# Kernel optimization log

Hardware: AMD Instinct MI355X
Metric: run time of the kernel (lower is better)

The kernel has to match this reference:

```python
import jax, jax.numpy as jnp
import numpy as np

LN_EPS = 1e-5

def setup_inputs() -> dict:
    key = jax.random.key(0)
    k1, k2, k3 = jax.random.split(key, 3)
    B, S, D = 4, 4096, 768
    seq_feat = jax.random.normal(k1, (B, S, D), dtype=jnp.float32)
    msa_feat = jax.random.normal(k2, (B, S, D), dtype=jnp.float32)
    ln_gamma = jnp.ones((2 * D,), dtype=jnp.float32)
    ln_beta = jnp.zeros((2 * D,), dtype=jnp.float32)
    # torch init zeroes gate weight; use small random weights for a non-degenerate test
    gate_w = jax.random.normal(k3, (2, 2 * D), dtype=jnp.float32) * 0.02
    gate_b = jnp.zeros((2,), dtype=jnp.float32)
    return {"seq_feat": seq_feat, "msa_feat": msa_feat, "ln_gamma": ln_gamma,
            "ln_beta": ln_beta, "gate_w": gate_w, "gate_b": gate_b}

def reference(seq_feat, msa_feat, ln_gamma, ln_beta, gate_w, gate_b):
    # h: [B, S, 2D]
    h = jnp.concatenate([seq_feat, msa_feat], axis=-1)
    mean = jnp.mean(h, axis=-1, keepdims=True)
    var = jnp.mean(jnp.square(h - mean), axis=-1, keepdims=True)
    hn = (h - mean) * jax.lax.rsqrt(var + LN_EPS) * ln_gamma + ln_beta
    # dropout in eval mode = identity
    logits = jnp.einsum('bsd,kd->bsk', hn, gate_w) + gate_b  # [B, S, 2]
    w = jax.nn.softmax(logits, axis=-1)
    return w[..., 0:1] * seq_feat + w[..., 1:2] * msa_feat
```

## Files before the change

### kernel.cpp

```cpp
#include <hip/hip_runtime.h>

#define LN_EPS 1e-5f
#define D 768
#define D4 192
#define TWO_D 1536


__global__ __launch_bounds__(64) void setup_kernel(
    const float* __restrict__ gamma, const float* __restrict__ beta,
    const float* __restrict__ gate_w, const float* __restrict__ gate_b,
    float* __restrict__ ws)
{
    const int lane = threadIdx.x;
    const float4* g4  = (const float4*)gamma;
    const float4* b4  = (const float4*)beta;
    const float4* w04 = (const float4*)gate_w;
    const float4* w14 = (const float4*)(gate_w + TWO_D);
    float4* P04 = (float4*)ws;
    float4* P14 = (float4*)(ws + TWO_D);

    float C0 = 0.f, C1 = 0.f, E0 = 0.f, E1 = 0.f;
    #pragma unroll
    for (int j = 0; j < 6; ++j) {
        const int idx = j * 64 + lane;
        float4 g = g4[idx], bb = b4[idx], w0 = w04[idx], w1 = w14[idx];
        float4 p0, p1;
        p0.x = g.x * w0.x; p0.y = g.y * w0.y; p0.z = g.z * w0.z; p0.w = g.w * w0.w;
        p1.x = g.x * w1.x; p1.y = g.y * w1.y; p1.z = g.z * w1.z; p1.w = g.w * w1.w;
        P04[idx] = p0;
        P14[idx] = p1;
        C0 += p0.x + p0.y + p0.z + p0.w;
        C1 += p1.x + p1.y + p1.z + p1.w;
        E0 += bb.x * w0.x + bb.y * w0.y + bb.z * w0.z + bb.w * w0.w;
        E1 += bb.x * w1.x + bb.y * w1.y + bb.z * w1.z + bb.w * w1.w;
    }
    #pragma unroll
    for (int off = 32; off > 0; off >>= 1) {
        C0 += __shfl_xor(C0, off, 64);
        C1 += __shfl_xor(C1, off, 64);
        E0 += __shfl_xor(E0, off, 64);
        E1 += __shfl_xor(E1, off, 64);
    }
    if (lane == 0) {
        float* c = ws + 2 * TWO_D;
        c[0] = C0;
        c[1] = C1;
        c[2] = E0 + gate_b[0];
        c[3] = E1 + gate_b[1];
    }
}

__global__ __launch_bounds__(256) void fused_gate_kernel(
    const float* __restrict__ seq, const float* __restrict__ msa,
    const float* __restrict__ ws, float* __restrict__ out, int nrows)
{
    const int wave = threadIdx.x >> 6;
    const int lane = threadIdx.x & 63;
    const int row = blockIdx.x * 4 + wave;
    if (row >= nrows) return;

    const float4* s4 = (const float4*)(seq + (size_t)row * D);
    const float4* m4 = (const float4*)(msa + (size_t)row * D);
    const float4* P04 = (const float4*)ws;
    const float4* P14 = (const float4*)(ws + TWO_D);

    float4 s[3], m[3];
    #pragma unroll
    for (int j = 0; j < 3; ++j) {
        s[j] = s4[j * 64 + lane];
        m[j] = m4[j * 64 + lane];
    }
    const float4 cst = *(const float4*)(ws + 2 * TWO_D);

    float su = 0.f, sq = 0.f, a0 = 0.f, a1 = 0.f;
    #pragma unroll
    for (int j = 0; j < 6; ++j) {
        const int idx = (j < 3) ? (j * 64 + lane) : (D4 + (j - 3) * 64 + lane);
        const float4 p0 = P04[idx];
        const float4 p1 = P14[idx];
        const float4 h = (j < 3) ? s[j] : m[j - 3];
        su += h.x + h.y + h.z + h.w;
        sq += h.x * h.x + h.y * h.y + h.z * h.z + h.w * h.w;
        a0 += h.x * p0.x + h.y * p0.y + h.z * p0.z + h.w * p0.w;
        a1 += h.x * p1.x + h.y * p1.y + h.z * p1.z + h.w * p1.w;
    }
    #pragma unroll
    for (int off = 32; off > 0; off >>= 1) {
        su += __shfl_xor(su, off, 64);
        sq += __shfl_xor(sq, off, 64);
        a0 += __shfl_xor(a0, off, 64);
        a1 += __shfl_xor(a1, off, 64);
    }

    const float inv_n = 1.f / (float)TWO_D;
    const float mean = su * inv_n;
    const float var  = fmaxf(sq * inv_n - mean * mean, 0.f);
    const float rstd = rsqrtf(var + LN_EPS);
    const float l0 = rstd * (a0 - mean * cst.x) + cst.z;
    const float l1 = rstd * (a1 - mean * cst.y) + cst.w;
    const float mx = fmaxf(l0, l1);
    const float e0 = __expf(l0 - mx), e1 = __expf(l1 - mx);
    const float inv = 1.f / (e0 + e1);
    const float w0s = e0 * inv, w1s = e1 * inv;

    float4* o4 = (float4*)(out + (size_t)row * D);
    #pragma unroll
    for (int j = 0; j < 3; ++j) {
        float4 o;
        o.x = w0s * s[j].x + w1s * m[j].x;
        o.y = w0s * s[j].y + w1s * m[j].y;
        o.z = w0s * s[j].z + w1s * m[j].z;
        o.w = w0s * s[j].w + w1s * m[j].w;
        o4[j * 64 + lane] = o;
    }
}

extern "C" void kernel_launch(void* const* d_in, const int* in_sizes, int n_in,
                              void* d_out, int out_size, void* d_ws, size_t ws_size,
                              hipStream_t stream) {
    const float* seq    = (const float*)d_in[0];
    const float* msa    = (const float*)d_in[1];
    const float* gamma  = (const float*)d_in[2];
    const float* beta   = (const float*)d_in[3];
    const float* gate_w = (const float*)d_in[4];
    const float* gate_b = (const float*)d_in[5];
    float* out = (float*)d_out;
    float* ws  = (float*)d_ws;

    const int nrows = in_sizes[0] / D;
    setup_kernel<<<1, 64, 0, stream>>>(gamma, beta, gate_w, gate_b, ws);
    fused_gate_kernel<<<(nrows + 3) / 4, 256, 0, stream>>>(seq, msa, ws, out, nrows);
}
```

Before: 146.4 us.

## Use persistent grid-stride waves with next-row prefetch, LDS-staged gate weights, nontemporal I/O

The main kernel becomes persistent. It launches 1024 blocks, and each wave walks rows with a grid stride, prefetching the next row's seq and msa data into registers while it processes the current row. The folded gate weights and constants are copied once per block into shared memory instead of being re-read from global memory for every row. Row loads and output stores use nontemporal hints to avoid polluting the cache. This adds register pressure from the double buffer and a per-block LDS prologue and barrier, and a fixed grid size may leave CUs unevenly loaded.

```diff
diff --git a/kernel.cpp b/kernel.cpp
--- a/kernel.cpp
+++ b/kernel.cpp
@@ -4,6 +4,8 @@
 #define D 768
 #define D4 192
 #define TWO_D 1536
+
+typedef float f4 __attribute__((ext_vector_type(4)));
 
 
 __global__ __launch_bounds__(64) void setup_kernel(
@@ -12,21 +14,20 @@
     float* __restrict__ ws)
 {
     const int lane = threadIdx.x;
-    const float4* g4  = (const float4*)gamma;
-    const float4* b4  = (const float4*)beta;
-    const float4* w04 = (const float4*)gate_w;
-    const float4* w14 = (const float4*)(gate_w + TWO_D);
-    float4* P04 = (float4*)ws;
-    float4* P14 = (float4*)(ws + TWO_D);
+    const f4* g4  = (const f4*)gamma;
+    const f4* b4  = (const f4*)beta;
+    const f4* w04 = (const f4*)gate_w;
+    const f4* w14 = (const f4*)(gate_w + TWO_D);
+    f4* P04 = (f4*)ws;
+    f4* P14 = (f4*)(ws + TWO_D);
 
     float C0 = 0.f, C1 = 0.f, E0 = 0.f, E1 = 0.f;
     #pragma unroll
     for (int j = 0; j < 6; ++j) {
         const int idx = j * 64 + lane;
-        float4 g = g4[idx], bb = b4[idx], w0 = w04[idx], w1 = w14[idx];
-        float4 p0, p1;
-        p0.x = g.x * w0.x; p0.y = g.y * w0.y; p0.z = g.z * w0.z; p0.w = g.w * w0.w;
-        p1.x = g.x * w1.x; p1.y = g.y * w1.y; p1.z = g.z * w1.z; p1.w = g.w * w1.w;
+        f4 g = g4[idx], bb = b4[idx], w0 = w04[idx], w1 = w14[idx];
+        f4 p0 = g * w0;
+        f4 p1 = g * w1;
         P04[idx] = p0;
         P14[idx] = p1;
         C0 += p0.x + p0.y + p0.z + p0.w;
@@ -52,66 +53,102 @@
 
 __global__ __launch_bounds__(256) void fused_gate_kernel(
     const float* __restrict__ seq, const float* __restrict__ msa,
-    const float* __restrict__ ws, float* __restrict__ out, int nrows)
+    const float* __restrict__ ws, float* __restrict__ out,
+    int nrows, int nwaves)
 {
+    __shared__ float ldsbuf[2 * TWO_D + 4];
+
+    {
+        const f4* w4 = (const f4*)ws;
+        f4* l4 = (f4*)ldsbuf;
+        #pragma unroll
+        for (int t = 0; t < 3; ++t)
+            l4[threadIdx.x + t * 256] = w4[threadIdx.x + t * 256];
+        if (threadIdx.x < 4)
+            ldsbuf[2 * TWO_D + threadIdx.x] = ws[2 * TWO_D + threadIdx.x];
+    }
+    __syncthreads();
+
     const int wave = threadIdx.x >> 6;
     const int lane = threadIdx.x & 63;
-    const int row = blockIdx.x * 4 + wave;
-    if (row >= nrows) return;
+    int r = blockIdx.x * 4 + wave;
+    if (r >= nrows) return;
 
-    const float4* s4 = (const float4*)(seq + (size_t)row * D);
-    const float4* m4 = (const float4*)(msa + (size_t)row * D);
-    const float4* P04 = (const float4*)ws;
-    const float4* P14 = (const float4*)(ws + TWO_D);
+    const f4* P0l = (const f4*)ldsbuf;
+    const f4* P1l = (const f4*)(ldsbuf + TWO_D);
+    const float C0c = ldsbuf[2 * TWO_D + 0];
+    const float C1c = ldsbuf[2 * TWO_D + 1];
+    const float E0c = ldsbuf[2 * TWO_D + 2];
+    const float E1c = ldsbuf[2 * TWO_D + 3];
+    const float inv_n = 1.f / (float)TWO_D;
 
-    float4 s[3], m[3];
-    #pragma unroll
-    for (int j = 0; j < 3; ++j) {
-        s[j] = s4[j * 64 + lane];
-        m[j] = m4[j * 64 + lane];
-    }
-    const float4 cst = *(const float4*)(ws + 2 * TWO_D);
-
-    float su = 0.f, sq = 0.f, a0 = 0.f, a1 = 0.f;
-    #pragma unroll
-    for (int j = 0; j < 6; ++j) {
-        const int idx = (j < 3) ? (j * 64 + lane) : (D4 + (j - 3) * 64 + lane);
-        const float4 p0 = P04[idx];
-        const float4 p1 = P14[idx];
-        const float4 h = (j < 3) ? s[j] : m[j - 3];
-        su += h.x + h.y + h.z + h.w;
-        sq += h.x * h.x + h.y * h.y + h.z * h.z + h.w * h.w;
-        a0 += h.x * p0.x + h.y * p0.y + h.z * p0.z + h.w * p0.w;
-        a1 += h.x * p1.x + h.y * p1.y + h.z * p1.z + h.w * p1.w;
-    }
-    #pragma unroll
-    for (int off = 32; off > 0; off >>= 1) {
-        su += __shfl_xor(su, off, 64);
-        sq += __shfl_xor(sq, off, 64);
-        a0 += __shfl_xor(a0, off, 64);
-        a1 += __shfl_xor(a1, off, 64);
+    f4 s[3], m[3];
+    {
+        const f4* sp = (const f4*)(seq + (size_t)r * D);
+        const f4* mp = (const f4*)(msa + (size_t)r * D);
+        #pragma unroll
+        for (int j = 0; j < 3; ++j) {
+            s[j] = __builtin_nontemporal_load(&sp[j * 64 + lane]);
+            m[j] = __builtin_nontemporal_load(&mp[j * 64 + lane]);
+        }
     }
 
-    const float inv_n = 1.f / (float)TWO_D;
-    const float mean = su * inv_n;
-    const float var  = fmaxf(sq * inv_n - mean * mean, 0.f);
-    const float rstd = rsqrtf(var + LN_EPS);
-    const float l0 = rstd * (a0 - mean * cst.x) + cst.z;
-    const float l1 = rstd * (a1 - mean * cst.y) + cst.w;
-    const float mx = fmaxf(l0, l1);
-    const float e0 = __expf(l0 - mx), e1 = __expf(l1 - mx);
-    const float inv = 1.f / (e0 + e1);
-    const float w0s = e0 * inv, w1s = e1 * inv;
+    for (;;) {
+        const int rn = r + nwaves;
+        const bool more = rn < nrows;
 
-    float4* o4 = (float4*)(out + (size_t)row * D);
-    #pragma unroll
-    for (int j = 0; j < 3; ++j) {
-        float4 o;
-        o.x = w0s * s[j].x + w1s * m[j].x;
-        o.y = w0s * s[j].y + w1s * m[j].y;
-        o.z = w0s * s[j].z + w1s * m[j].z;
-        o.w = w0s * s[j].w + w1s * m[j].w;
-        o4[j * 64 + lane] = o;
+        f4 ns[3], nm[3];
+        if (more) {
+            const f4* snp = (const f4*)(seq + (size_t)rn * D);
+            const f4* mnp = (const f4*)(msa + (size_t)rn * D);
+            #pragma unroll
+            for (int j = 0; j < 3; ++j) {
+                ns[j] = __builtin_nontemporal_load(&snp[j * 64 + lane]);
+                nm[j] = __builtin_nontemporal_load(&mnp[j * 64 + lane]);
+            }
+        }
+
+        float su = 0.f, sq = 0.f, a0 = 0.f, a1 = 0.f;
+        #pragma unroll
+        for (int j = 0; j < 6; ++j) {
+            const int idx = (j < 3) ? (j * 64 + lane) : (D4 + (j - 3) * 64 + lane);
+            const f4 p0 = P0l[idx];
+            const f4 p1 = P1l[idx];
+            const f4 h = (j < 3) ? s[j] : m[j - 3];
+            su += h.x + h.y + h.z + h.w;
+            sq += h.x * h.x + h.y * h.y + h.z * h.z + h.w * h.w;
+            a0 += h.x * p0.x + h.y * p0.y + h.z * p0.z + h.w * p0.w;
+            a1 += h.x * p1.x + h.y * p1.y + h.z * p1.z + h.w * p1.w;
+        }
+        #pragma unroll
+        for (int off = 32; off > 0; off >>= 1) {
+            su += __shfl_xor(su, off, 64);
+            sq += __shfl_xor(sq, off, 64);
+            a0 += __shfl_xor(a0, off, 64);
+            a1 += __shfl_xor(a1, off, 64);
+        }
+
+        const float mean = su * inv_n;
+        const float var  = fmaxf(sq * inv_n - mean * mean, 0.f);
+        const float rstd = rsqrtf(var + LN_EPS);
+        const float l0 = rstd * (a0 - mean * C0c) + E0c;
+        const float l1 = rstd * (a1 - mean * C1c) + E1c;
+        const float mx = fmaxf(l0, l1);
+        const float e0 = __expf(l0 - mx), e1 = __expf(l1 - mx);
+        const float inv = 1.f / (e0 + e1);
+        const float w0s = e0 * inv, w1s = e1 * inv;
+
+        f4* o4 = (f4*)(out + (size_t)r * D);
+        #pragma unroll
+        for (int j = 0; j < 3; ++j) {
+            f4 o = w0s * s[j] + w1s * m[j];
+            __builtin_nontemporal_store(o, &o4[j * 64 + lane]);
+        }
+
+        if (!more) break;
+        #pragma unroll
+        for (int j = 0; j < 3; ++j) { s[j] = ns[j]; m[j] = nm[j]; }
+        r = rn;
     }
 }
 
@@ -129,5 +166,7 @@
 
     const int nrows = in_sizes[0] / D;
     setup_kernel<<<1, 64, 0, stream>>>(gamma, beta, gate_w, gate_b, ws);
-    fused_gate_kernel<<<(nrows + 3) / 4, 256, 0, stream>>>(seq, msa, ws, out, nrows);
+    const int blocks = 1024;
+    const int nwaves = blocks * 4;
+    fused_gate_kernel<<<blocks, 256, 0, stream>>>(seq, msa, ws, out, nrows, nwaves);
 }
```

Measured after the change: 148.2 us. No clear change (+1.2%).

## Fold gate-weight setup into main kernel and process four rows per wave

Applied to the files above, without the earlier changes.

Removes the separate single-block setup kernel by having each wave recompute gamma*gate_w products and bias constants inline, which drops one launch and the serial dependency between the two kernels. Each wave now handles four rows, so those parameter loads and the constant reductions are shared across the rows. Row loads and output stores use nontemporal hints. The cost is higher register pressure from holding 24 float4 values per lane, which may reduce occupancy, plus redundant per-wave parameter reads.

```diff
diff --git a/kernel.cpp b/kernel.cpp
--- a/kernel.cpp
+++ b/kernel.cpp
@@ -4,114 +4,108 @@
 #define D 768
 #define D4 192
 #define TWO_D 1536
+#define RPW 4
 
+typedef float f4 __attribute__((ext_vector_type(4)));
 
-__global__ __launch_bounds__(64) void setup_kernel(
+__global__ __launch_bounds__(256) void fused_gate_kernel(
+    const float* __restrict__ seq, const float* __restrict__ msa,
     const float* __restrict__ gamma, const float* __restrict__ beta,
     const float* __restrict__ gate_w, const float* __restrict__ gate_b,
-    float* __restrict__ ws)
+    float* __restrict__ out, int nrows)
 {
-    const int lane = threadIdx.x;
-    const float4* g4  = (const float4*)gamma;
-    const float4* b4  = (const float4*)beta;
-    const float4* w04 = (const float4*)gate_w;
-    const float4* w14 = (const float4*)(gate_w + TWO_D);
-    float4* P04 = (float4*)ws;
-    float4* P14 = (float4*)(ws + TWO_D);
+    const int wave = threadIdx.x >> 6;
+    const int lane = threadIdx.x & 63;
+    const int base = (blockIdx.x * 4 + wave) * RPW;
+    if (base >= nrows) return;
+
+    int rr[RPW];
+    bool valid[RPW];
+    #pragma unroll
+    for (int i = 0; i < RPW; ++i) {
+        const int r = base + i;
+        valid[i] = (r < nrows);
+        rr[i] = valid[i] ? r : (nrows - 1);
+    }
+
+    f4 s[RPW][3], m[RPW][3];
+    #pragma unroll
+    for (int i = 0; i < RPW; ++i) {
+        const f4* sp = (const f4*)(seq + (size_t)rr[i] * D);
+        const f4* mp = (const f4*)(msa + (size_t)rr[i] * D);
+        #pragma unroll
+        for (int j = 0; j < 3; ++j) {
+            s[i][j] = __builtin_nontemporal_load(&sp[j * 64 + lane]);
+            m[i][j] = __builtin_nontemporal_load(&mp[j * 64 + lane]);
+        }
+    }
+
+    const f4* g4  = (const f4*)gamma;
+    const f4* b4  = (const f4*)beta;
+    const f4* w04 = (const f4*)gate_w;
+    const f4* w14 = (const f4*)(gate_w + TWO_D);
 
     float C0 = 0.f, C1 = 0.f, E0 = 0.f, E1 = 0.f;
+    float su[RPW], sq[RPW], a0[RPW], a1[RPW];
+    #pragma unroll
+    for (int i = 0; i < RPW; ++i) { su[i] = sq[i] = a0[i] = a1[i] = 0.f; }
+
     #pragma unroll
     for (int j = 0; j < 6; ++j) {
-        const int idx = j * 64 + lane;
-        float4 g = g4[idx], bb = b4[idx], w0 = w04[idx], w1 = w14[idx];
-        float4 p0, p1;
-        p0.x = g.x * w0.x; p0.y = g.y * w0.y; p0.z = g.z * w0.z; p0.w = g.w * w0.w;
-        p1.x = g.x * w1.x; p1.y = g.y * w1.y; p1.z = g.z * w1.z; p1.w = g.w * w1.w;
-        P04[idx] = p0;
-        P14[idx] = p1;
+        const int idx = (j < 3) ? (j * 64 + lane) : (D4 + (j - 3) * 64 + lane);
+        const f4 g = g4[idx], bb = b4[idx], w0 = w04[idx], w1 = w14[idx];
+        const f4 p0 = g * w0;
+        const f4 p1 = g * w1;
         C0 += p0.x + p0.y + p0.z + p0.w;
         C1 += p1.x + p1.y + p1.z + p1.w;
         E0 += bb.x * w0.x + bb.y * w0.y + bb.z * w0.z + bb.w * w0.w;
         E1 += bb.x * w1.x + bb.y * w1.y + bb.z * w1.z + bb.w * w1.w;
+        #pragma unroll
+        for (int i = 0; i < RPW; ++i) {
+            const f4 h = (j < 3) ? s[i][j] : m[i][j - 3];
+            su[i] += h.x + h.y + h.z + h.w;
+            sq[i] += h.x * h.x + h.y * h.y + h.z * h.z + h.w * h.w;
+            a0[i] += h.x * p0.x + h.y * p0.y + h.z * p0.z + h.w * p0.w;
+            a1[i] += h.x * p1.x + h.y * p1.y + h.z * p1.z + h.w * p1.w;
+        }
     }
+
     #pragma unroll
     for (int off = 32; off > 0; off >>= 1) {
         C0 += __shfl_xor(C0, off, 64);
         C1 += __shfl_xor(C1, off, 64);
         E0 += __shfl_xor(E0, off, 64);
         E1 += __shfl_xor(E1, off, 64);
-    }
-    if (lane == 0) {
-        float* c = ws + 2 * TWO_D;
-        c[0] = C0;
-        c[1] = C1;
-        c[2] = E0 + gate_b[0];
-        c[3] = E1 + gate_b[1];
-    }
-}
-
-__global__ __launch_bounds__(256) void fused_gate_kernel(
-    const float* __restrict__ seq, const float* __restrict__ msa,
-    const float* __restrict__ ws, float* __restrict__ out, int nrows)
-{
-    const int wave = threadIdx.x >> 6;
-    const int lane = threadIdx.x & 63;
-    const int row = blockIdx.x * 4 + wave;
-    if (row >= nrows) return;
-
-    const float4* s4 = (const float4*)(seq + (size_t)row * D);
-    const float4* m4 = (const float4*)(msa + (size_t)row * D);
-    const float4* P04 = (const float4*)ws;
-    const float4* P14 = (const float4*)(ws + TWO_D);
-
-    float4 s[3], m[3];
-    #pragma unroll
-    for (int j = 0; j < 3; ++j) {
-        s[j] = s4[j * 64 + lane];
-        m[j] = m4[j * 64 + lane];
-    }
-    const float4 cst = *(const float4*)(ws + 2 * TWO_D);
-
-    float su = 0.f, sq = 0.f, a0 = 0.f, a1 = 0.f;
-    #pragma unroll
-    for (int j = 0; j < 6; ++j) {
-        const int idx = (j < 3) ? (j * 64 + lane) : (D4 + (j - 3) * 64 + lane);
-        const float4 p0 = P04[idx];
-        const float4 p1 = P14[idx];
-        const float4 h = (j < 3) ? s[j] : m[j - 3];
-        su += h.x + h.y + h.z + h.w;
-        sq += h.x * h.x + h.y * h.y + h.z * h.z + h.w * h.w;
-        a0 += h.x * p0.x + h.y * p0.y + h.z * p0.z + h.w * p0.w;
-        a1 += h.x * p1.x + h.y * p1.y + h.z * p1.z + h.w * p1.w;
-    }
-    #pragma unroll
-    for (int off = 32; off > 0; off >>= 1) {
-        su += __shfl_xor(su, off, 64);
-        sq += __shfl_xor(sq, off, 64);
-        a0 += __shfl_xor(a0, off, 64);
-        a1 += __shfl_xor(a1, off, 64);
+        #pragma unroll
+        for (int i = 0; i < RPW; ++i) {
+            su[i] += __shfl_xor(su[i], off, 64);
+            sq[i] += __shfl_xor(sq[i], off, 64);
+            a0[i] += __shfl_xor(a0[i], off, 64);
+            a1[i] += __shfl_xor(a1[i], off, 64);
+        }
     }
 
+    const float gb0 = gate_b[0], gb1 = gate_b[1];
     const float inv_n = 1.f / (float)TWO_D;
-    const float mean = su * inv_n;
-    const float var  = fmaxf(sq * inv_n - mean * mean, 0.f);
-    const float rstd = rsqrtf(var + LN_EPS);
-    const float l0 = rstd * (a0 - mean * cst.x) + cst.z;
-    const float l1 = rstd * (a1 - mean * cst.y) + cst.w;
-    const float mx = fmaxf(l0, l1);
-    const float e0 = __expf(l0 - mx), e1 = __expf(l1 - mx);
-    const float inv = 1.f / (e0 + e1);
-    const float w0s = e0 * inv, w1s = e1 * inv;
 
-    float4* o4 = (float4*)(out + (size_t)row * D);
     #pragma unroll
-    for (int j = 0; j < 3; ++j) {
-        float4 o;
-        o.x = w0s * s[j].x + w1s * m[j].x;
-        o.y = w0s * s[j].y + w1s * m[j].y;
-        o.z = w0s * s[j].z + w1s * m[j].z;
-        o.w = w0s * s[j].w + w1s * m[j].w;
-        o4[j * 64 + lane] = o;
+    for (int i = 0; i < RPW; ++i) {
+        if (!valid[i]) continue;
+        const float mean = su[i] * inv_n;
+        const float var  = fmaxf(sq[i] * inv_n - mean * mean, 0.f);
+        const float rstd = rsqrtf(var + LN_EPS);
+        const float l0 = rstd * (a0[i] - mean * C0) + E0 + gb0;
+        const float l1 = rstd * (a1[i] - mean * C1) + E1 + gb1;
+        const float mx = fmaxf(l0, l1);
+        const float e0 = __expf(l0 - mx), e1 = __expf(l1 - mx);
+        const float inv = 1.f / (e0 + e1);
+        const float w0s = e0 * inv, w1s = e1 * inv;
+        f4* o4 = (f4*)(out + (size_t)rr[i] * D);
+        #pragma unroll
+        for (int j = 0; j < 3; ++j) {
+            f4 o = w0s * s[i][j] + w1s * m[i][j];
+            __builtin_nontemporal_store(o, &o4[j * 64 + lane]);
+        }
     }
 }
 
@@ -125,9 +119,10 @@
     const float* gate_w = (const float*)d_in[4];
     const float* gate_b = (const float*)d_in[5];
     float* out = (float*)d_out;
-    float* ws  = (float*)d_ws;
 
     const int nrows = in_sizes[0] / D;
-    setup_kernel<<<1, 64, 0, stream>>>(gamma, beta, gate_w, gate_b, ws);
-    fused_gate_kernel<<<(nrows + 3) / 4, 256, 0, stream>>>(seq, msa, ws, out, nrows);
+    const int rows_per_block = 4 * RPW;
+    const int blocks = (nrows + rows_per_block - 1) / rows_per_block;
+    fused_gate_kernel<<<blocks, 256, 0, stream>>>(
+        seq, msa, gamma, beta, gate_w, gate_b, out, nrows);
 }
```

Result: no change. 147.6 us (+0.8%).

## Split fused gate kernel into stats pass and persistent blend pass

Applied to the files above, without the earlier changes.

Splits the single fused kernel in two. The first kernel computes per-row LayerNorm statistics and folded gate constants inline, replacing the separate setup kernel, and writes the softmax weights per row. The second is a grid-strided blend kernel that handles two rows per wave and writes output with nontemporal stores. The fused kernel read seq and msa once; this version reads them twice, which adds about 100MB of traffic in exchange for a simpler streaming write phase. Every wave now also recomputes the gamma/beta/weight products, which adds redundant loads and ALU work.

```diff
diff --git a/kernel.cpp b/kernel.cpp
--- a/kernel.cpp
+++ b/kernel.cpp
@@ -5,80 +5,47 @@
 #define D4 192
 #define TWO_D 1536
 
+typedef float f4 __attribute__((ext_vector_type(4)));
 
-__global__ __launch_bounds__(64) void setup_kernel(
+__global__ __launch_bounds__(256) void stats_kernel(
+    const float* __restrict__ seq, const float* __restrict__ msa,
     const float* __restrict__ gamma, const float* __restrict__ beta,
     const float* __restrict__ gate_w, const float* __restrict__ gate_b,
-    float* __restrict__ ws)
-{
-    const int lane = threadIdx.x;
-    const float4* g4  = (const float4*)gamma;
-    const float4* b4  = (const float4*)beta;
-    const float4* w04 = (const float4*)gate_w;
-    const float4* w14 = (const float4*)(gate_w + TWO_D);
-    float4* P04 = (float4*)ws;
-    float4* P14 = (float4*)(ws + TWO_D);
-
-    float C0 = 0.f, C1 = 0.f, E0 = 0.f, E1 = 0.f;
-    #pragma unroll
-    for (int j = 0; j < 6; ++j) {
-        const int idx = j * 64 + lane;
-        float4 g = g4[idx], bb = b4[idx], w0 = w04[idx], w1 = w14[idx];
-        float4 p0, p1;
-        p0.x = g.x * w0.x; p0.y = g.y * w0.y; p0.z = g.z * w0.z; p0.w = g.w * w0.w;
-        p1.x = g.x * w1.x; p1.y = g.y * w1.y; p1.z = g.z * w1.z; p1.w = g.w * w1.w;
-        P04[idx] = p0;
-        P14[idx] = p1;
-        C0 += p0.x + p0.y + p0.z + p0.w;
-        C1 += p1.x + p1.y + p1.z + p1.w;
-        E0 += bb.x * w0.x + bb.y * w0.y + bb.z * w0.z + bb.w * w0.w;
-        E1 += bb.x * w1.x + bb.y * w1.y + bb.z * w1.z + bb.w * w1.w;
-    }
-    #pragma unroll
-    for (int off = 32; off > 0; off >>= 1) {
-        C0 += __shfl_xor(C0, off, 64);
-        C1 += __shfl_xor(C1, off, 64);
-        E0 += __shfl_xor(E0, off, 64);
-        E1 += __shfl_xor(E1, off, 64);
-    }
-    if (lane == 0) {
-        float* c = ws + 2 * TWO_D;
-        c[0] = C0;
-        c[1] = C1;
-        c[2] = E0 + gate_b[0];
-        c[3] = E1 + gate_b[1];
-    }
-}
-
-__global__ __launch_bounds__(256) void fused_gate_kernel(
-    const float* __restrict__ seq, const float* __restrict__ msa,
-    const float* __restrict__ ws, float* __restrict__ out, int nrows)
+    float* __restrict__ gate_ws, int nrows)
 {
     const int wave = threadIdx.x >> 6;
     const int lane = threadIdx.x & 63;
     const int row = blockIdx.x * 4 + wave;
     if (row >= nrows) return;
 
-    const float4* s4 = (const float4*)(seq + (size_t)row * D);
-    const float4* m4 = (const float4*)(msa + (size_t)row * D);
-    const float4* P04 = (const float4*)ws;
-    const float4* P14 = (const float4*)(ws + TWO_D);
+    const f4* sp = (const f4*)(seq + (size_t)row * D);
+    const f4* mp = (const f4*)(msa + (size_t)row * D);
 
-    float4 s[3], m[3];
+    f4 s[3], m[3];
     #pragma unroll
     for (int j = 0; j < 3; ++j) {
-        s[j] = s4[j * 64 + lane];
-        m[j] = m4[j * 64 + lane];
+        s[j] = sp[j * 64 + lane];
+        m[j] = mp[j * 64 + lane];
     }
-    const float4 cst = *(const float4*)(ws + 2 * TWO_D);
+
+    const f4* g4  = (const f4*)gamma;
+    const f4* b4  = (const f4*)beta;
+    const f4* w04 = (const f4*)gate_w;
+    const f4* w14 = (const f4*)(gate_w + TWO_D);
 
     float su = 0.f, sq = 0.f, a0 = 0.f, a1 = 0.f;
+    float C0 = 0.f, C1 = 0.f, E0 = 0.f, E1 = 0.f;
     #pragma unroll
     for (int j = 0; j < 6; ++j) {
         const int idx = (j < 3) ? (j * 64 + lane) : (D4 + (j - 3) * 64 + lane);
-        const float4 p0 = P04[idx];
-        const float4 p1 = P14[idx];
-        const float4 h = (j < 3) ? s[j] : m[j - 3];
+        const f4 g = g4[idx], bb = b4[idx], w0 = w04[idx], w1 = w14[idx];
+        const f4 p0 = g * w0;
+        const f4 p1 = g * w1;
+        C0 += p0.x + p0.y + p0.z + p0.w;
+        C1 += p1.x + p1.y + p1.z + p1.w;
+        E0 += bb.x * w0.x + bb.y * w0.y + bb.z * w0.z + bb.w * w0.w;
+        E1 += bb.x * w1.x + bb.y * w1.y + bb.z * w1.z + bb.w * w1.w;
+        const f4 h = (j < 3) ? s[j] : m[j - 3];
         su += h.x + h.y + h.z + h.w;
         sq += h.x * h.x + h.y * h.y + h.z * h.z + h.w * h.w;
         a0 += h.x * p0.x + h.y * p0.y + h.z * p0.z + h.w * p0.w;
@@ -90,28 +57,73 @@
         sq += __shfl_xor(sq, off, 64);
         a0 += __shfl_xor(a0, off, 64);
         a1 += __shfl_xor(a1, off, 64);
+        C0 += __shfl_xor(C0, off, 64);
+        C1 += __shfl_xor(C1, off, 64);
+        E0 += __shfl_xor(E0, off, 64);
+        E1 += __shfl_xor(E1, off, 64);
     }
 
-    const float inv_n = 1.f / (float)TWO_D;
-    const float mean = su * inv_n;
-    const float var  = fmaxf(sq * inv_n - mean * mean, 0.f);
-    const float rstd = rsqrtf(var + LN_EPS);
-    const float l0 = rstd * (a0 - mean * cst.x) + cst.z;
-    const float l1 = rstd * (a1 - mean * cst.y) + cst.w;
-    const float mx = fmaxf(l0, l1);
-    const float e0 = __expf(l0 - mx), e1 = __expf(l1 - mx);
-    const float inv = 1.f / (e0 + e1);
-    const float w0s = e0 * inv, w1s = e1 * inv;
+    if (lane == 0) {
+        const float inv_n = 1.f / (float)TWO_D;
+        const float mean = su * inv_n;
+        const float var  = fmaxf(sq * inv_n - mean * mean, 0.f);
+        const float rstd = rsqrtf(var + LN_EPS);
+        const float l0 = rstd * (a0 - mean * C0) + E0 + gate_b[0];
+        const float l1 = rstd * (a1 - mean * C1) + E1 + gate_b[1];
+        const float mx = fmaxf(l0, l1);
+        const float e0 = __expf(l0 - mx), e1 = __expf(l1 - mx);
+        const float inv = 1.f / (e0 + e1);
+        float2 w;
+        w.x = e0 * inv;
+        w.y = e1 * inv;
+        ((float2*)gate_ws)[row] = w;
+    }
+}
 
-    float4* o4 = (float4*)(out + (size_t)row * D);
-    #pragma unroll
-    for (int j = 0; j < 3; ++j) {
-        float4 o;
-        o.x = w0s * s[j].x + w1s * m[j].x;
-        o.y = w0s * s[j].y + w1s * m[j].y;
-        o.z = w0s * s[j].z + w1s * m[j].z;
-        o.w = w0s * s[j].w + w1s * m[j].w;
-        o4[j * 64 + lane] = o;
+__global__ __launch_bounds__(256) void blend_kernel(
+    const float* __restrict__ seq, const float* __restrict__ msa,
+    const float* __restrict__ gate_ws, float* __restrict__ out,
+    int nrows, int nwaves)
+{
+    const int lane = threadIdx.x & 63;
+    const int wid  = (int)((blockIdx.x * blockDim.x + threadIdx.x) >> 6);
+    const float2* gw = (const float2*)gate_ws;
+
+    for (int base = wid * 2; base < nrows; base += nwaves * 2) {
+        const int r0 = base;
+        const bool has1 = (base + 1) < nrows;
+        const int r1 = has1 ? (base + 1) : base;
+
+        const f4* s0p = (const f4*)(seq + (size_t)r0 * D);
+        const f4* m0p = (const f4*)(msa + (size_t)r0 * D);
+        const f4* s1p = (const f4*)(seq + (size_t)r1 * D);
+        const f4* m1p = (const f4*)(msa + (size_t)r1 * D);
+
+        const float2 w0 = gw[r0];
+        const float2 w1 = gw[r1];
+        f4 s0[3], m0[3], s1[3], m1[3];
+        #pragma unroll
+        for (int j = 0; j < 3; ++j) {
+            s0[j] = s0p[j * 64 + lane];
+            m0[j] = m0p[j * 64 + lane];
+            s1[j] = s1p[j * 64 + lane];
+            m1[j] = m1p[j * 64 + lane];
+        }
+
+        f4* o0 = (f4*)(out + (size_t)r0 * D);
+        #pragma unroll
+        for (int j = 0; j < 3; ++j) {
+            f4 o = w0.x * s0[j] + w0.y * m0[j];
+            __builtin_nontemporal_store(o, &o0[j * 64 + lane]);
+        }
+        if (has1) {
+            f4* o1 = (f4*)(out + (size_t)r1 * D);
+            #pragma unroll
+            for (int j = 0; j < 3; ++j) {
+                f4 o = w1.x * s1[j] + w1.y * m1[j];
+                __builtin_nontemporal_store(o, &o1[j * 64 + lane]);
+            }
+        }
     }
 }
 
@@ -128,6 +140,9 @@
     float* ws  = (float*)d_ws;
 
     const int nrows = in_sizes[0] / D;
-    setup_kernel<<<1, 64, 0, stream>>>(gamma, beta, gate_w, gate_b, ws);
-    fused_gate_kernel<<<(nrows + 3) / 4, 256, 0, stream>>>(seq, msa, ws, out, nrows);
+    stats_kernel<<<(nrows + 3) / 4, 256, 0, stream>>>(
+        seq, msa, gamma, beta, gate_w, gate_b, ws, nrows);
+    const int blocks = 2048;
+    const int nwaves = blocks * 4;
+    blend_kernel<<<blocks, 256, 0, stream>>>(seq, msa, ws, out, nrows, nwaves);
 }
```

Result: slower. 163.4 us (+11.6%).
